# Kernel tuning notes

Hardware: AMD Instinct MI355X
Metric: run time of the kernel (lower is better)

## Reference

```python
import jax, jax.numpy as jnp
import numpy as np

ALPHA = 0.2   # LeakyReLU negative slope
OF = 64       # out_features


def setup_inputs() -> dict:
    key = jax.random.key(0)
    k1, k2, k3, k4 = jax.random.split(key, 4)
    h = jax.random.normal(k1, (16, 2048, 12, 128), dtype=jnp.float32)
    adj = jax.random.randint(k2, (2, 6, 6), 0, 2, dtype=jnp.int32)
    # learned params (xavier-like scale)
    W = jax.random.normal(k3, (128, 64), dtype=jnp.float32) * 0.1
    a = jax.random.normal(k4, (2, 2 * OF, 1), dtype=jnp.float32) * 0.1
    return {"h": h, "adj": adj, "W": W, "a": a}


def reference(h, adj, W, a):
    # h: [B, N, 12, Fin], adj: [2, 6, 6], W: [Fin, OF], a: [2, 2*OF, 1]
    Wh = jnp.einsum('bnkf,fo->bnko', h, W)  # [B, N, 12, OF]
    outs = []
    for i in range(2):  # fixed 2 chunks of 6 nodes (h.shape[2] // 6)
        chunk = Wh[:, :, i * 6:(i + 1) * 6, :]       # [B, N, 6, OF]
        # matmul(a_input, a[i]) decomposes: e_pq = a1.Wh_p + a2.Wh_q
        a1 = a[i, :OF, 0]
        a2 = a[i, OF:, 0]
        s1 = chunk @ a1                               # [B, N, 6]
        s2 = chunk @ a2                               # [B, N, 6]
        e = jax.nn.leaky_relu(s1[..., :, None] + s2[..., None, :], ALPHA)  # [B,N,6,6]
        ei = e[i]                                     # NOTE: batch index i, as in source
        att = jnp.where(adj[i] > 0, ei, jnp.float32(-9e15))  # [N, 6, 6]
        att = jax.nn.softmax(att, axis=-1)
        # dropout omitted (eval mode)
        outs.append(jnp.einsum('npq,bnqf->bnpf', att, chunk))  # [B, N, 6, OF]
    h_prime = jnp.concatenate(outs, axis=2)           # [B, N, 12, OF]
    return jax.nn.elu(h_prime)                        # concat=True -> ELU
```

## Files before the change

### kernel.cpp

```cpp
#include <hip/hip_runtime.h>
#include <math.h>

#define LRELU_ALPHA 0.2f
#define NEG_BIG -9000000000000000.0f

typedef __attribute__((ext_vector_type(8))) short bf16x8;
typedef __attribute__((ext_vector_type(4))) float f32x4;

static __device__ inline unsigned short f2bf(float x) {
    unsigned int u = __float_as_uint(x);
    unsigned int r = (u + 0x7FFFu + ((u >> 16) & 1u)) >> 16;
    return (unsigned short)r;
}

__global__ __launch_bounds__(256) void gat_att_kernel(
    const float* __restrict__ h, const int* __restrict__ adj,
    const float* __restrict__ W, const float* __restrict__ a,
    float* __restrict__ att_ws)
{
    __shared__ float sm[4 * 6 * 128];
    const int warp = threadIdx.x >> 6;
    const int lane = threadIdx.x & 63;
    const int iw = blockIdx.x * 4 + warp;
    const int gi = iw >> 11;
    const int n  = iw & 2047;

    const float* hp = h + ((size_t)(gi * 2048 + n) * 12 + (size_t)gi * 6) * 128;
    float* smw = sm + warp * 768;

#pragma unroll
    for (int j = 0; j < 3; ++j)
        *(float4*)(smw + j * 256 + lane * 4) = *(const float4*)(hp + j * 256 + lane * 4);
    __syncthreads();

    const int f = lane;
    float acc[6];
#pragma unroll
    for (int q = 0; q < 6; ++q) acc[q] = 0.f;

    const float* Wp = W + f;
    for (int c = 0; c < 128; c += 4) {
        float w0 = Wp[(c + 0) * 64];
        float w1 = Wp[(c + 1) * 64];
        float w2 = Wp[(c + 2) * 64];
        float w3 = Wp[(c + 3) * 64];
#pragma unroll
        for (int q = 0; q < 6; ++q) {
            float4 hv = *(const float4*)(smw + q * 128 + c);
            acc[q] = fmaf(hv.x, w0, fmaf(hv.y, w1, fmaf(hv.z, w2, fmaf(hv.w, w3, acc[q]))));
        }
    }

    const float a1v = a[gi * 128 + f];
    const float a2v = a[gi * 128 + 64 + f];
    float s1[6], s2[6];
#pragma unroll
    for (int q = 0; q < 6; ++q) {
        float t1 = acc[q] * a1v;
        float t2 = acc[q] * a2v;
#pragma unroll
        for (int off = 32; off > 0; off >>= 1) {
            t1 += __shfl_xor(t1, off, 64);
            t2 += __shfl_xor(t2, off, 64);
        }
        s1[q] = t1;
        s2[q] = t2;
    }

    if (lane < 6) {
        const int p = lane;
        float s1p = s1[0];
#pragma unroll
        for (int q = 1; q < 6; ++q) { if (p == q) s1p = s1[q]; }

        float row[6];
        float mx = -3.0e38f;
#pragma unroll
        for (int q = 0; q < 6; ++q) {
            float e = s1p + s2[q];
            e = (e > 0.f) ? e : (LRELU_ALPHA * e);
            const int ad = adj[gi * 36 + p * 6 + q];
            const float m = (ad > 0) ? e : NEG_BIG;
            row[q] = m;
            mx = fmaxf(mx, m);
        }
        float sum = 0.f;
#pragma unroll
        for (int q = 0; q < 6; ++q) {
            row[q] = expf(row[q] - mx);
            sum += row[q];
        }
        const float inv = 1.f / sum;
        float* op = att_ws + (size_t)iw * 36 + p * 6;
#pragma unroll
        for (int q = 0; q < 6; ++q) op[q] = row[q] * inv;
    }
}

__global__ __launch_bounds__(256) void gat_main_mfma(
    const float* __restrict__ h, const float* __restrict__ W,
    const float* __restrict__ att_ws, float* __restrict__ out)
{
    __shared__ __align__(16) short lds[32768];
    short* Wt = lds;
    const int tid  = threadIdx.x;
    const int warp = tid >> 6;
    const int lane = tid & 63;
    short* Pw = lds + 8192 + warp * 6144;

    for (int idx = tid; idx < 8192; idx += 256) {
        const int k = idx >> 6, n = idx & 63;
        Wt[n * 128 + k] = (short)f2bf(W[idx]);
    }

    const int wave_id = blockIdx.x * 4 + warp;
    const int bn0 = wave_id * 4;
    const int half = lane >> 5;
    const int li   = lane & 31;

    for (int pair = 0; pair < 2; ++pair) {
        const int bno = pair * 2 + half;
        const int bn  = bn0 + bno;
        const int n   = bn & 2047;

        const float* hb = h + (size_t)bn * 1536 + li * 4;
        float4 hv[12];
#pragma unroll
        for (int r = 0; r < 12; ++r)
            hv[r] = *(const float4*)(hb + r * 128);

#pragma unroll
        for (int gi = 0; gi < 2; ++gi) {
            const float4* ap = (const float4*)(att_ws + (size_t)(gi * 2048 + n) * 36);
            float4 av[9];
#pragma unroll
            for (int j = 0; j < 9; ++j) av[j] = ap[j];
            float attv[36];
#pragma unroll
            for (int j = 0; j < 9; ++j) {
                attv[j * 4 + 0] = av[j].x; attv[j * 4 + 1] = av[j].y;
                attv[j * 4 + 2] = av[j].z; attv[j * 4 + 3] = av[j].w;
            }
#pragma unroll
            for (int p = 0; p < 6; ++p) {
                float ax = 0.f, ay = 0.f, az = 0.f, aw = 0.f;
#pragma unroll
                for (int q = 0; q < 6; ++q) {
                    const float apq = attv[p * 6 + q];
                    const float4 hq = hv[gi * 6 + q];
                    ax = fmaf(apq, hq.x, ax);
                    ay = fmaf(apq, hq.y, ay);
                    az = fmaf(apq, hq.z, az);
                    aw = fmaf(apq, hq.w, aw);
                }
                const int row = bno * 12 + gi * 6 + p;
                ushort4 pk;
                pk.x = f2bf(ax); pk.y = f2bf(ay);
                pk.z = f2bf(az); pk.w = f2bf(aw);
                *(ushort4*)(Pw + row * 128 + li * 4) = pk;
            }
        }
    }
    __syncthreads();

    const int col  = lane & 15;
    const int quad = lane >> 4;
    f32x4 acc[3][4];
#pragma unroll
    for (int mt = 0; mt < 3; ++mt)
#pragma unroll
        for (int nt = 0; nt < 4; ++nt)
            acc[mt][nt] = (f32x4){0.f, 0.f, 0.f, 0.f};

#pragma unroll
    for (int ks = 0; ks < 4; ++ks) {
        bf16x8 bfr[4];
#pragma unroll
        for (int nt = 0; nt < 4; ++nt)
            bfr[nt] = *(const bf16x8*)(Wt + (nt * 16 + col) * 128 + ks * 32 + quad * 8);
#pragma unroll
        for (int mt = 0; mt < 3; ++mt) {
            bf16x8 afr = *(const bf16x8*)(Pw + (mt * 16 + col) * 128 + ks * 32 + quad * 8);
#pragma unroll
            for (int nt = 0; nt < 4; ++nt)
                acc[mt][nt] = __builtin_amdgcn_mfma_f32_16x16x32_bf16(
                    afr, bfr[nt], acc[mt][nt], 0, 0, 0);
        }
    }

    float* ob = out + (size_t)bn0 * 12 * 64;
#pragma unroll
    for (int mt = 0; mt < 3; ++mt)
#pragma unroll
        for (int nt = 0; nt < 4; ++nt)
#pragma unroll
            for (int r = 0; r < 4; ++r) {
                const int row = mt * 16 + quad * 4 + r;
                float v = acc[mt][nt][r];
                v = (v > 0.f) ? v : (expf(v) - 1.f);
                ob[row * 64 + nt * 16 + col] = v;
            }
}

extern "C" void kernel_launch(void* const* d_in, const int* in_sizes, int n_in,
                              void* d_out, int out_size, void* d_ws, size_t ws_size,
                              hipStream_t stream) {
    const float* h   = (const float*)d_in[0];
    const int*   adj = (const int*)d_in[1];
    const float* W   = (const float*)d_in[2];
    const float* a   = (const float*)d_in[3];
    float* out = (float*)d_out;
    float* att_ws = (float*)d_ws;

    hipLaunchKernelGGL(gat_att_kernel, dim3(1024), dim3(256), 0, stream,
                       h, adj, W, a, att_ws);
    hipLaunchKernelGGL(gat_main_mfma, dim3(2048), dim3(256), 0, stream,
                       h, W, att_ws, out);
}
```

Before: 340.1 us.

## Precompute W·a vectors and bf16 W in prep kernel; simplify attention scores

```diff
diff --git a/kernel.cpp b/kernel.cpp
--- a/kernel.cpp
+++ b/kernel.cpp
@@ -3,6 +3,9 @@
 
 #define LRELU_ALPHA 0.2f
 #define NEG_BIG -9000000000000000.0f
+
+#define WA_OFF 147456
+#define WF_OFF 147968
 
 typedef __attribute__((ext_vector_type(8))) short bf16x8;
 typedef __attribute__((ext_vector_type(4))) float f32x4;
@@ -13,71 +16,72 @@
     return (unsigned short)r;
 }
 
+__global__ __launch_bounds__(256) void gat_prep_kernel(
+    const float* __restrict__ W, const float* __restrict__ a,
+    float* __restrict__ ws)
+{
+    const int tid = threadIdx.x;
+    if (blockIdx.x < 32) {
+        short* wf = (short*)(ws + WF_OFF);
+        const int o = blockIdx.x * 256 + tid;
+        const int n = o >> 7, k = o & 127;
+        wf[o] = (short)f2bf(W[k * 64 + n]);
+    } else {
+        float* wa = ws + WA_OFF;
+        for (int idx = tid; idx < 512; idx += 256) {
+            const int gi = idx >> 8, j = (idx >> 7) & 1, c = idx & 127;
+            const float* Wr = W + c * 64;
+            const float* ar = a + gi * 128 + j * 64;
+            float s = 0.f;
+#pragma unroll
+            for (int f = 0; f < 64; ++f) s = fmaf(Wr[f], ar[f], s);
+            wa[idx] = s;
+        }
+    }
+}
+
 __global__ __launch_bounds__(256) void gat_att_kernel(
     const float* __restrict__ h, const int* __restrict__ adj,
-    const float* __restrict__ W, const float* __restrict__ a,
-    float* __restrict__ att_ws)
+    float* __restrict__ ws)
 {
-    __shared__ float sm[4 * 6 * 128];
     const int warp = threadIdx.x >> 6;
     const int lane = threadIdx.x & 63;
     const int iw = blockIdx.x * 4 + warp;
     const int gi = iw >> 11;
     const int n  = iw & 2047;
 
-    const float* hp = h + ((size_t)(gi * 2048 + n) * 12 + (size_t)gi * 6) * 128;
-    float* smw = sm + warp * 768;
-
-#pragma unroll
-    for (int j = 0; j < 3; ++j)
-        *(float4*)(smw + j * 256 + lane * 4) = *(const float4*)(hp + j * 256 + lane * 4);
-    __syncthreads();
-
-    const int f = lane;
-    float acc[6];
-#pragma unroll
-    for (int q = 0; q < 6; ++q) acc[q] = 0.f;
-
-    const float* Wp = W + f;
-    for (int c = 0; c < 128; c += 4) {
-        float w0 = Wp[(c + 0) * 64];
-        float w1 = Wp[(c + 1) * 64];
-        float w2 = Wp[(c + 2) * 64];
-        float w3 = Wp[(c + 3) * 64];
+    const float* wa = ws + WA_OFF;
+    const float2 w1 = *(const float2*)(wa + gi * 256 + 2 * lane);
+    const float2 w2 = *(const float2*)(wa + gi * 256 + 128 + 2 * lane);
+    const float* hp = h + ((size_t)(gi * 2048 + n) * 12 + (size_t)gi * 6) * 128 + 2 * lane;
+
+    float t1[6], t2[6];
+#pragma unroll
+    for (int q = 0; q < 6; ++q) {
+        const float2 hq = *(const float2*)(hp + q * 128);
+        t1[q] = hq.x * w1.x + hq.y * w1.y;
+        t2[q] = hq.x * w2.x + hq.y * w2.y;
+    }
+#pragma unroll
+    for (int off = 32; off > 0; off >>= 1) {
 #pragma unroll
         for (int q = 0; q < 6; ++q) {
-            float4 hv = *(const float4*)(smw + q * 128 + c);
-            acc[q] = fmaf(hv.x, w0, fmaf(hv.y, w1, fmaf(hv.z, w2, fmaf(hv.w, w3, acc[q]))));
-        }
-    }
-
-    const float a1v = a[gi * 128 + f];
-    const float a2v = a[gi * 128 + 64 + f];
-    float s1[6], s2[6];
-#pragma unroll
-    for (int q = 0; q < 6; ++q) {
-        float t1 = acc[q] * a1v;
-        float t2 = acc[q] * a2v;
-#pragma unroll
-        for (int off = 32; off > 0; off >>= 1) {
-            t1 += __shfl_xor(t1, off, 64);
-            t2 += __shfl_xor(t2, off, 64);
-        }
-        s1[q] = t1;
-        s2[q] = t2;
+            t1[q] += __shfl_xor(t1[q], off, 64);
+            t2[q] += __shfl_xor(t2[q], off, 64);
+        }
     }
 
     if (lane < 6) {
         const int p = lane;
-        float s1p = s1[0];
-#pragma unroll
-        for (int q = 1; q < 6; ++q) { if (p == q) s1p = s1[q]; }
+        float s1p = t1[0];
+#pragma unroll
+        for (int q = 1; q < 6; ++q) { if (p == q) s1p = t1[q]; }
 
         float row[6];
         float mx = -3.0e38f;
 #pragma unroll
         for (int q = 0; q < 6; ++q) {
-            float e = s1p + s2[q];
+            float e = s1p + t2[q];
             e = (e > 0.f) ? e : (LRELU_ALPHA * e);
             const int ad = adj[gi * 36 + p * 6 + q];
             const float m = (ad > 0) ? e : NEG_BIG;
@@ -91,27 +95,22 @@
             sum += row[q];
         }
         const float inv = 1.f / sum;
-        float* op = att_ws + (size_t)iw * 36 + p * 6;
+        float* op = ws + (size_t)iw * 36 + p * 6;
 #pragma unroll
         for (int q = 0; q < 6; ++q) op[q] = row[q] * inv;
     }
 }
 
+#define PSTR 136
 __global__ __launch_bounds__(256) void gat_main_mfma(
-    const float* __restrict__ h, const float* __restrict__ W,
-    const float* __restrict__ att_ws, float* __restrict__ out)
+    const float* __restrict__ h, const float* __restrict__ ws,
+    float* __restrict__ out)
 {
-    __shared__ __align__(16) short lds[32768];
-    short* Wt = lds;
+    __shared__ __align__(16) short lds[4 * 48 * PSTR];
     const int tid  = threadIdx.x;
     const int warp = tid >> 6;
     const int lane = tid & 63;
-    short* Pw = lds + 8192 + warp * 6144;
-
-    for (int idx = tid; idx < 8192; idx += 256) {
-        const int k = idx >> 6, n = idx & 63;
-        Wt[n * 128 + k] = (short)f2bf(W[idx]);
-    }
+    short* Pw = lds + warp * 48 * PSTR;
 
     const int wave_id = blockIdx.x * 4 + warp;
     const int bn0 = wave_id * 4;
@@ -131,15 +130,13 @@
 
 #pragma unroll
         for (int gi = 0; gi < 2; ++gi) {
-            const float4* ap = (const float4*)(att_ws + (size_t)(gi * 2048 + n) * 36);
-            float4 av[9];
-#pragma unroll
-            for (int j = 0; j < 9; ++j) av[j] = ap[j];
+            const float4* ap = (const float4*)(ws + (size_t)(gi * 2048 + n) * 36);
             float attv[36];
 #pragma unroll
             for (int j = 0; j < 9; ++j) {
-                attv[j * 4 + 0] = av[j].x; attv[j * 4 + 1] = av[j].y;
-                attv[j * 4 + 2] = av[j].z; attv[j * 4 + 3] = av[j].w;
+                const float4 av = ap[j];
+                attv[j * 4 + 0] = av.x; attv[j * 4 + 1] = av.y;
+                attv[j * 4 + 2] = av.z; attv[j * 4 + 3] = av.w;
             }
 #pragma unroll
             for (int p = 0; p < 6; ++p) {
@@ -157,12 +154,12 @@
                 ushort4 pk;
                 pk.x = f2bf(ax); pk.y = f2bf(ay);
                 pk.z = f2bf(az); pk.w = f2bf(aw);
-                *(ushort4*)(Pw + row * 128 + li * 4) = pk;
+                *(ushort4*)(Pw + row * PSTR + li * 4) = pk;
             }
         }
     }
-    __syncthreads();
-
+
+    const short* wf = (const short*)(ws + WF_OFF);
     const int col  = lane & 15;
     const int quad = lane >> 4;
     f32x4 acc[3][4];
@@ -177,18 +174,20 @@
         bf16x8 bfr[4];
 #pragma unroll
         for (int nt = 0; nt < 4; ++nt)
-            bfr[nt] = *(const bf16x8*)(Wt + (nt * 16 + col) * 128 + ks * 32 + quad * 8);
-#pragma unroll
-        for (int mt = 0; mt < 3; ++mt) {
-            bf16x8 afr = *(const bf16x8*)(Pw + (mt * 16 + col) * 128 + ks * 32 + quad * 8);
+            bfr[nt] = *(const bf16x8*)(wf + (nt * 16 + col) * 128 + ks * 32 + quad * 8);
+        bf16x8 afr[3];
+#pragma unroll
+        for (int mt = 0; mt < 3; ++mt)
+            afr[mt] = *(const bf16x8*)(Pw + (mt * 16 + col) * PSTR + ks * 32 + quad * 8);
+#pragma unroll
+        for (int mt = 0; mt < 3; ++mt)
 #pragma unroll
             for (int nt = 0; nt < 4; ++nt)
                 acc[mt][nt] = __builtin_amdgcn_mfma_f32_16x16x32_bf16(
-                    afr, bfr[nt], acc[mt][nt], 0, 0, 0);
-        }
-    }
-
-    float* ob = out + (size_t)bn0 * 12 * 64;
+                    afr[mt], bfr[nt], acc[mt][nt], 0, 0, 0);
+    }
+
+    float* ob = out + (size_t)bn0 * 768;
 #pragma unroll
     for (int mt = 0; mt < 3; ++mt)
 #pragma unroll
@@ -210,10 +209,9 @@
     const float* W   = (const float*)d_in[2];
     const float* a   = (const float*)d_in[3];
     float* out = (float*)d_out;
-    float* att_ws = (float*)d_ws;
-
-    hipLaunchKernelGGL(gat_att_kernel, dim3(1024), dim3(256), 0, stream,
-                       h, adj, W, a, att_ws);
-    hipLaunchKernelGGL(gat_main_mfma, dim3(2048), dim3(256), 0, stream,
-                       h, W, att_ws, out);
-}
+    float* ws  = (float*)d_ws;
+
+    hipLaunchKernelGGL(gat_prep_kernel, dim3(33), dim3(256), 0, stream, W, a, ws);
+    hipLaunchKernelGGL(gat_att_kernel, dim3(1024), dim3(256), 0, stream, h, adj, ws);
+    hipLaunchKernelGGL(gat_main_mfma, dim3(2048), dim3(256), 0, stream, h, ws, out);
+}
```

Measured after the change: 331.0 us. -2.7%, faster.
